# Optimization experiments

Measured on AMD Instinct MI355X. Metric: run time of the kernel, lower is better.

Reference implementation:

```python
import jax, jax.numpy as jnp
import numpy as np

B, S, D_IN, D_OUT = 4, 2048, 1024, 1024

def setup_inputs() -> dict:
    key = jax.random.key(0)
    kx, kq, kk, kv = jax.random.split(key, 4)
    sc = 1.0 / np.sqrt(D_IN)
    x = jax.random.normal(kx, (B, S, D_IN), dtype=jnp.float32)
    Wq = jax.random.normal(kq, (D_IN, D_OUT), dtype=jnp.float32) * sc
    Wk = jax.random.normal(kk, (D_IN, D_OUT), dtype=jnp.float32) * sc
    Wv = jax.random.normal(kv, (D_IN, D_OUT), dtype=jnp.float32) * sc
    return {"x": x, "Wq": Wq, "Wk": Wk, "Wv": Wv}

def reference(x, Wq, Wk, Wv):
    # x: [B,S,Din]; projections to [B,S,Dout]
    q = jnp.einsum('bsd,de->bse', x, Wq)
    k = jnp.einsum('bsd,de->bse', x, Wk)
    v = jnp.einsum('bsd,de->bse', x, Wv)
    scale = 1.0 / jnp.sqrt(jnp.asarray(q.shape[-1], q.dtype))
    scores = jnp.einsum('bqe,bke->bqk', q, k) * scale  # [B,S,S]
    causal = jnp.tril(jnp.ones((scores.shape[-2], scores.shape[-1]), dtype=bool))
    scores = jnp.where(causal, scores, -jnp.inf)
    attn = jax.nn.softmax(scores, axis=-1)
    # dropout p=0.0 -> identity
    return jnp.einsum('bqk,bke->bqe', attn, v)
```

## Files before the change

### kernel.cpp

```cpp
#include <hip/hip_runtime.h>

#define SEQ 2048
#define DIM 1024

typedef __attribute__((ext_vector_type(8))) __bf16 bf16x8;
typedef __attribute__((ext_vector_type(4))) float f32x4;

typedef __attribute__((address_space(1))) unsigned char gu8_t;
typedef __attribute__((address_space(3))) unsigned char lu8_t;

__device__ __forceinline__ void async_copy16(const void* g, void* l) {
  __builtin_amdgcn_global_load_lds((gu8_t*)g, (lu8_t*)l, 16, 0, 0);
}

__device__ __forceinline__ ushort f2bf(float f) {
  union { float f; unsigned u; } v;
  v.f = f;
  unsigned r = v.u + 0x7FFFu + ((v.u >> 16) & 1u);
  return (ushort)(r >> 16);
}

__global__ void detect_and_zero(const unsigned* __restrict__ words,
                                int* __restrict__ flag,
                                float* __restrict__ lsum) {
  const int t = threadIdx.x;
  for (int i = t; i < 4 * SEQ; i += 256) lsum[i] = 0.0f;
  if (t < 64) {
    int hits = 0;
    for (int i = 0; i < 64; i++) {
      const unsigned w = words[t * 64 + i];
      const unsigned b = (w >> 8) & 0x7Fu;
      hits += (b >= 0x3Bu && b <= 0x42u) ? 1 : 0;
    }
#pragma unroll
    for (int o = 32; o > 0; o >>= 1) hits += __shfl_xor(hits, o, 64);
    if (t == 0) *flag = (hits > 2048) ? 1 : 0;
  }
}

__global__ void prep(const void* __restrict__ xin, const void* __restrict__ w0,
                     const void* __restrict__ w1, const void* __restrict__ w2,
                     ushort* __restrict__ xb, ushort* __restrict__ wt,
                     const int* __restrict__ flag) {
  __shared__ ushort tile[64][68];
  const int bid = blockIdx.x;
  const int t = threadIdx.x;
  const int bf = *flag;

  if (bid < 4096) {
    const int i = bid * 256 + t;
    if (bf) {
      reinterpret_cast<uint4*>(xb)[i] =
          reinterpret_cast<const uint4*>(xin)[i];
    } else {
      const float4* f = reinterpret_cast<const float4*>(xin);
      const float4 a = f[2 * i], b = f[2 * i + 1];
      ushort4 lo, hi;
      lo.x = f2bf(a.x); lo.y = f2bf(a.y); lo.z = f2bf(a.z); lo.w = f2bf(a.w);
      hi.x = f2bf(b.x); hi.y = f2bf(b.y); hi.z = f2bf(b.z); hi.w = f2bf(b.w);
      reinterpret_cast<ushort4*>(xb)[2 * i] = lo;
      reinterpret_cast<ushort4*>(xb)[2 * i + 1] = hi;
    }
    return;
  }

  const int rem = bid - 4096;
  const int z = rem >> 8;
  const int within = rem & 255;
  const int c0 = (within & 15) * 64, r0 = (within >> 4) * 64;
  const void* in = (z == 0) ? w0 : (z == 1) ? w1 : w2;
  ushort* op = wt + (size_t)z * 1024 * 1024;

  if (bf) {
    const ushort* ip = (const ushort*)in;
#pragma unroll
    for (int i = 0; i < 4; i++) {
      const int lin = i * 256 + t;
      const int r = lin >> 4, c4 = (lin & 15) << 2;
      const ushort4 v = *reinterpret_cast<const ushort4*>(
          ip + (size_t)(r0 + r) * 1024 + c0 + c4);
      tile[r][c4 + 0] = v.x; tile[r][c4 + 1] = v.y;
      tile[r][c4 + 2] = v.z; tile[r][c4 + 3] = v.w;
    }
  } else {
    const float* ip = (const float*)in;
#pragma unroll
    for (int i = 0; i < 4; i++) {
      const int lin = i * 256 + t;
      const int r = lin >> 4, c4 = (lin & 15) << 2;
      const float4 v = *reinterpret_cast<const float4*>(
          ip + (size_t)(r0 + r) * 1024 + c0 + c4);
      tile[r][c4 + 0] = f2bf(v.x); tile[r][c4 + 1] = f2bf(v.y);
      tile[r][c4 + 2] = f2bf(v.z); tile[r][c4 + 3] = f2bf(v.w);
    }
  }
  __syncthreads();
#pragma unroll
  for (int i = 0; i < 4; i++) {
    const int lin = i * 256 + t;
    const int c = lin >> 4, r4 = (lin & 15) << 2;
    ushort4 v;
    v.x = tile[r4 + 0][c]; v.y = tile[r4 + 1][c];
    v.z = tile[r4 + 2][c]; v.w = tile[r4 + 3][c];
    *reinterpret_cast<ushort4*>(op + (size_t)(c0 + c) * 1024 + r0 + r4) = v;
  }
}

template <int EPI, int OUTK, int TRI, int CK, int CBAL, int SWIZ, int M,
          int N, int K, long AZ, long BZ, long CZ, long BRS>
__global__ __launch_bounds__(256, 4) void gemm_t(
    const ushort* __restrict__ A, const ushort* __restrict__ Bt,
    void* __restrict__ Cv, const int* __restrict__ flag,
    float* __restrict__ lsum, float scale0, float scale1) {
  __shared__ ushort lA[128 * 64];
  __shared__ ushort lB[128 * 64];
  __shared__ float lsh[(EPI == 2) ? 128 : 1];

  constexpr int MT = M / 128;
  const int nT = gridDim.x;
  const int id = blockIdx.y * nT + blockIdx.x;
  const int xcd = id & 7;
  const int loc = id >> 3;
  int nt, mt;
  if constexpr (SWIZ == 1) {
    const int ng = nT >> 3;
    nt = xcd * ng + loc % ng;
    mt = loc / ng;
  } else {
    nt = loc % nT;
    const int s = loc / nT;
    if constexpr (CBAL) {
      mt = (s == 0) ? xcd : (MT - 1 - xcd);
    } else {
      mt = xcd + (s << 3);
    }
  }
  const int n0 = nt * 128;
  const int m0 = mt * 128;
  if (TRI && n0 > m0 + 127) return;

  const int z = blockIdx.z;
  const ushort* Ab = A + (size_t)z * AZ;
  const ushort* Bb = Bt + (size_t)z * BZ;

  const int t = threadIdx.x;
  const int lane = t & 63;
  const int w = t >> 6;
  const int wm = (w >> 1) * 64;
  const int wn = (w & 1) * 64;
  const int quad = lane >> 4;
  const int l15 = lane & 15;

  if constexpr (EPI == 2) {
    if (t < 128) lsh[t] = 1.0f / lsum[(size_t)z * M + m0 + t];
  }

  f32x4 acc[4][4] = {};

  const int kEnd = CK ? ((m0 + 128 < K) ? (m0 + 128) : K) : K;

  for (int k0 = 0; k0 < kEnd; k0 += 64) {
    __syncthreads();
#pragma unroll
    for (int g0 = 0; g0 < 1024; g0 += 256) {
      const int g = g0 + t;
      const int r = g >> 3, c = (g & 7) << 3;
      async_copy16(Ab + (size_t)(m0 + r) * K + k0 + c, lA + g * 8);
    }
#pragma unroll
    for (int g0 = 0; g0 < 1024; g0 += 256) {
      const int g = g0 + t;
      const int r = g >> 3, c = (g & 7) << 3;
      async_copy16(Bb + (size_t)(n0 + r) * BRS + k0 + c, lB + g * 8);
    }
    __syncthreads();

#pragma unroll
    for (int h = 0; h < 2; h++) {
      bf16x8 af[4], bfr[4];
#pragma unroll
      for (int mi = 0; mi < 4; mi++)
        af[mi] = *(const bf16x8*)(lA + (wm + mi * 16 + l15) * 64 + h * 32 +
                                  quad * 8);
#pragma unroll
      for (int ni = 0; ni < 4; ni++)
        bfr[ni] = *(const bf16x8*)(lB + (wn + ni * 16 + l15) * 64 + h * 32 +
                                   quad * 8);
#pragma unroll
      for (int mi = 0; mi < 4; mi++)
#pragma unroll
        for (int ni = 0; ni < 4; ni++)
          acc[mi][ni] = __builtin_amdgcn_mfma_f32_16x16x32_bf16(
              af[mi], bfr[ni], acc[mi][ni], 0, 0, 0);
    }
  }

  const size_t zc = (size_t)z * CZ;

  if constexpr (EPI == 1) {
    ushort* C = (ushort*)Cv + zc;
    float* ls = lsum + (size_t)z * M;
#pragma unroll
    for (int mi = 0; mi < 4; mi++)
#pragma unroll
      for (int r = 0; r < 4; r++) {
        const int row = m0 + wm + mi * 16 + quad * 4 + r;
        float partial = 0.0f;
#pragma unroll
        for (int ni = 0; ni < 4; ni++) {
          const int col = n0 + wn + ni * 16 + l15;
          const float ev = (col <= row) ? __expf(acc[mi][ni][r]) : 0.0f;
          C[(size_t)row * N + col] = f2bf(ev);
          partial += ev;
        }
#pragma unroll
        for (int o = 1; o < 16; o <<= 1) partial += __shfl_xor(partial, o, 64);
        if (l15 == 0) atomicAdd(&ls[row], partial);
      }
    return;
  } else {
    const float scale = (z == 0) ? scale0 : scale1;
    const bool storeBf = (OUTK == 1) || (OUTK == 2 && *flag != 0);
#pragma unroll
    for (int mi = 0; mi < 4; mi++)
#pragma unroll
      for (int ni = 0; ni < 4; ni++)
#pragma unroll
        for (int r = 0; r < 4; r++) {
          const int lrow = wm + mi * 16 + quad * 4 + r;
          const int row = m0 + lrow;
          const int col = n0 + wn + ni * 16 + l15;
          const float sc = (EPI == 2) ? lsh[lrow] : scale;
          const float vv = acc[mi][ni][r] * sc;
          if (storeBf) {
            ushort* C = (ushort*)Cv + zc;
            C[(size_t)row * N + col] = f2bf(vv);
          } else {
            float* C = (float*)Cv + zc;
            C[(size_t)row * N + col] = vv;
          }
        }
  }
}

extern "C" void kernel_launch(void* const* d_in, const int* in_sizes, int n_in,
                              void* d_out, int out_size, void* d_ws,
                              size_t ws_size, hipStream_t stream) {
  char* ws = (char*)d_ws;
  const size_t MB = 1024 * 1024;
  int* flag = (int*)ws;
  ushort* wt = (ushort*)(ws + 1 * MB);
  ushort* xb = (ushort*)(ws + 7 * MB);
  ushort* q = (ushort*)(ws + 23 * MB);
  ushort* kk = (ushort*)(ws + 39 * MB);
  ushort* vt = (ushort*)(ws + 55 * MB);
  ushort* sc = (ushort*)(ws + 71 * MB);
  float* lsum = (float*)(ws + 103 * MB);
  (void)kk;

  detect_and_zero<<<dim3(1), 256, 0, stream>>>((const unsigned*)d_in[0], flag,
                                               lsum);

  prep<<<dim3(4864), 256, 0, stream>>>(d_in[0], d_in[1], d_in[2], d_in[3], xb,
                                       wt, flag);

  gemm_t<0, 1, 0, 0, 0, 0, 8192, 1024, 1024, 0L, 1024L * 1024, 8192L * 1024,
         1024L>
      <<<dim3(8, 64, 2), 256, 0, stream>>>(xb, wt, (void*)q, flag, nullptr,
                                           0.03125f, 1.0f);

  gemm_t<0, 1, 0, 0, 0, 1, 1024, 8192, 1024, 0L, 0L, 0L, 1024L>
      <<<dim3(64, 8, 1), 256, 0, stream>>>(wt + 2 * 1024 * 1024, xb,
                                           (void*)vt, flag, nullptr, 1.0f,
                                           1.0f);

  gemm_t<1, 1, 1, 0, 1, 0, 2048, 2048, 1024, (long)SEQ * DIM, (long)SEQ * DIM,
         (long)SEQ * SEQ, (long)DIM>
      <<<dim3(16, 16, 4), 256, 0, stream>>>(q, kk, (void*)sc, flag, lsum,
                                            1.0f, 1.0f);

  gemm_t<2, 2, 0, 1, 1, 0, 2048, 1024, 2048, (long)SEQ * SEQ, 2048L,
         (long)SEQ * DIM, 8192L>
      <<<dim3(8, 16, 4), 256, 0, stream>>>(sc, vt, d_out, flag, lsum, 1.0f,
                                           1.0f);
}
```

Baseline: 254.8 us.

## Fold detect/zero into prep and launch only causal tiles for QK^T

Removes the separate single-block detect_and_zero launch. Every prep block now recomputes the bf16 detection from the first 1024 words, and extra blocks zero lsum and write the flag. The QK^T grid is cut from 16x16 to 8x17 per batch with a paired swizzle (SWIZ 2), so only lower-triangular tiles are launched instead of launching all tiles and early-returning the upper half. The PV GEMM gets a fixed xcd-to-n mapping (SWIZ 3). The cost is redundant detection reads in every prep block and an extra block barrier.

New measurement: 244.0 us. -4.2%, faster.

```diff
diff --git a/kernel.cpp b/kernel.cpp
--- a/kernel.cpp
+++ b/kernel.cpp
@@ -20,32 +20,35 @@
   return (ushort)(r >> 16);
 }
 
-__global__ void detect_and_zero(const unsigned* __restrict__ words,
-                                int* __restrict__ flag,
-                                float* __restrict__ lsum) {
-  const int t = threadIdx.x;
-  for (int i = t; i < 4 * SEQ; i += 256) lsum[i] = 0.0f;
-  if (t < 64) {
-    int hits = 0;
-    for (int i = 0; i < 64; i++) {
-      const unsigned w = words[t * 64 + i];
-      const unsigned b = (w >> 8) & 0x7Fu;
-      hits += (b >= 0x3Bu && b <= 0x42u) ? 1 : 0;
-    }
-#pragma unroll
-    for (int o = 32; o > 0; o >>= 1) hits += __shfl_xor(hits, o, 64);
-    if (t == 0) *flag = (hits > 2048) ? 1 : 0;
-  }
-}
-
 __global__ void prep(const void* __restrict__ xin, const void* __restrict__ w0,
                      const void* __restrict__ w1, const void* __restrict__ w2,
                      ushort* __restrict__ xb, ushort* __restrict__ wt,
-                     const int* __restrict__ flag) {
+                     int* __restrict__ flag, float* __restrict__ lsum) {
   __shared__ ushort tile[64][68];
+  __shared__ int redi[4];
   const int bid = blockIdx.x;
   const int t = threadIdx.x;
-  const int bf = *flag;
+
+  const unsigned* words = (const unsigned*)xin;
+  int hits = 0;
+#pragma unroll
+  for (int i = 0; i < 4; i++) {
+    const unsigned wv = words[t * 4 + i];
+    const unsigned b = (wv >> 8) & 0x7Fu;
+    hits += (b >= 0x3Bu && b <= 0x42u) ? 1 : 0;
+  }
+#pragma unroll
+  for (int o = 32; o > 0; o >>= 1) hits += __shfl_xor(hits, o, 64);
+  if ((t & 63) == 0) redi[t >> 6] = hits;
+  __syncthreads();
+  const int bf = (redi[0] + redi[1] + redi[2] + redi[3] > 512) ? 1 : 0;
+
+  if (bid >= 4864) {
+    reinterpret_cast<float4*>(lsum)[(bid - 4864) * 256 + t] =
+        make_float4(0.f, 0.f, 0.f, 0.f);
+    if (bid == 4864 && t == 0) *flag = bf;
+    return;
+  }
 
   if (bid < 4096) {
     const int i = bid * 256 + t;
@@ -106,8 +109,8 @@
   }
 }
 
-template <int EPI, int OUTK, int TRI, int CK, int CBAL, int SWIZ, int M,
-          int N, int K, long AZ, long BZ, long CZ, long BRS>
+template <int EPI, int OUTK, int CK, int SWIZ, int M, int N, int K, long AZ,
+          long BZ, long CZ, long BRS>
 __global__ __launch_bounds__(256, 4) void gemm_t(
     const ushort* __restrict__ A, const ushort* __restrict__ Bt,
     void* __restrict__ Cv, const int* __restrict__ flag,
@@ -126,18 +129,18 @@
     const int ng = nT >> 3;
     nt = xcd * ng + loc % ng;
     mt = loc / ng;
+  } else if constexpr (SWIZ == 2) {
+    if (loc <= xcd) { mt = xcd; nt = loc; }
+    else { mt = MT - 1 - xcd; nt = loc - xcd - 1; }
+  } else if constexpr (SWIZ == 3) {
+    nt = xcd;
+    mt = loc;
   } else {
     nt = loc % nT;
-    const int s = loc / nT;
-    if constexpr (CBAL) {
-      mt = (s == 0) ? xcd : (MT - 1 - xcd);
-    } else {
-      mt = xcd + (s << 3);
-    }
+    mt = xcd + ((loc / nT) << 3);
   }
   const int n0 = nt * 128;
   const int m0 = mt * 128;
-  if (TRI && n0 > m0 + 127) return;
 
   const int z = blockIdx.z;
   const ushort* Ab = A + (size_t)z * AZ;
@@ -258,28 +261,24 @@
   float* lsum = (float*)(ws + 103 * MB);
   (void)kk;
 
-  detect_and_zero<<<dim3(1), 256, 0, stream>>>((const unsigned*)d_in[0], flag,
-                                               lsum);
-
-  prep<<<dim3(4864), 256, 0, stream>>>(d_in[0], d_in[1], d_in[2], d_in[3], xb,
-                                       wt, flag);
-
-  gemm_t<0, 1, 0, 0, 0, 0, 8192, 1024, 1024, 0L, 1024L * 1024, 8192L * 1024,
-         1024L>
+  prep<<<dim3(4872), 256, 0, stream>>>(d_in[0], d_in[1], d_in[2], d_in[3], xb,
+                                       wt, flag, lsum);
+
+  gemm_t<0, 1, 0, 0, 8192, 1024, 1024, 0L, 1024L * 1024, 8192L * 1024, 1024L>
       <<<dim3(8, 64, 2), 256, 0, stream>>>(xb, wt, (void*)q, flag, nullptr,
                                            0.03125f, 1.0f);
 
-  gemm_t<0, 1, 0, 0, 0, 1, 1024, 8192, 1024, 0L, 0L, 0L, 1024L>
+  gemm_t<0, 1, 0, 1, 1024, 8192, 1024, 0L, 0L, 0L, 1024L>
       <<<dim3(64, 8, 1), 256, 0, stream>>>(wt + 2 * 1024 * 1024, xb,
                                            (void*)vt, flag, nullptr, 1.0f,
                                            1.0f);
 
-  gemm_t<1, 1, 1, 0, 1, 0, 2048, 2048, 1024, (long)SEQ * DIM, (long)SEQ * DIM,
+  gemm_t<1, 1, 0, 2, 2048, 2048, 1024, (long)SEQ * DIM, (long)SEQ * DIM,
          (long)SEQ * SEQ, (long)DIM>
-      <<<dim3(16, 16, 4), 256, 0, stream>>>(q, kk, (void*)sc, flag, lsum,
-                                            1.0f, 1.0f);
-
-  gemm_t<2, 2, 0, 1, 1, 0, 2048, 1024, 2048, (long)SEQ * SEQ, 2048L,
+      <<<dim3(8, 17, 4), 256, 0, stream>>>(q, kk, (void*)sc, flag, lsum, 1.0f,
+                                           1.0f);
+
+  gemm_t<2, 2, 1, 3, 2048, 1024, 2048, (long)SEQ * SEQ, 2048L,
          (long)SEQ * DIM, 8192L>
       <<<dim3(8, 16, 4), 256, 0, stream>>>(sc, vt, d_out, flag, lsum, 1.0f,
                                            1.0f);
```
